# Kernel tuning notes

Measured on AMD Instinct MI355X. Metric: run time of the kernel, lower is better.

The kernel has to match this reference:

```python
import jax, jax.numpy as jnp
import numpy as np


def _conv(x, w, b, pad):
    y = jax.lax.conv_general_dilated(
        x, w, window_strides=(1, 1), padding=[(pad, pad), (pad, pad)],
        dimension_numbers=('NCHW', 'OIHW', 'NCHW'))
    return y + b[None, :, None, None]


def _deform_conv2d(x, offsets, mask, w, b):
    # x: [B,C,H,W]; offsets: [B,2*K,H,W] (dy,dx pairs per kernel tap, row-major taps);
    # mask: [B,K,H,W]; w: [O,C,3,3]; stride=1, padding=1 (torchvision semantics).
    B, C, H, W = x.shape
    K = 9
    off = offsets.reshape(B, K, 2, H, W)
    dy, dx = off[:, :, 0], off[:, :, 1]                      # [B,K,H,W]
    ky = (jnp.arange(K) // 3 - 1).astype(x.dtype)            # tap row offset (pad=1)
    kx = (jnp.arange(K) % 3 - 1).astype(x.dtype)             # tap col offset
    hh = jnp.arange(H, dtype=x.dtype)
    ww = jnp.arange(W, dtype=x.dtype)
    py = hh[None, None, :, None] + ky[None, :, None, None] + dy   # sample y, [B,K,H,W]
    px = ww[None, None, None, :] + kx[None, :, None, None] + dx   # sample x
    y0 = jnp.floor(py); x0 = jnp.floor(px)
    wy = py - y0;      wx = px - x0
    y0i = y0.astype(jnp.int32); x0i = x0.astype(jnp.int32)
    xflat = x.reshape(B, C, H * W)

    def gather(yy, xx):
        # zero padding outside the feature map (torchvision behavior)
        valid = ((yy >= 0) & (yy < H) & (xx >= 0) & (xx < W)).astype(x.dtype)
        idx = jnp.clip(yy, 0, H - 1) * W + jnp.clip(xx, 0, W - 1)
        idx = jnp.broadcast_to(idx.reshape(B, 1, K * H * W), (B, C, K * H * W))
        g = jnp.take_along_axis(xflat, idx, axis=2).reshape(B, C, K, H, W)
        return g * valid[:, None]

    sampled = (gather(y0i, x0i)         * ((1 - wy) * (1 - wx))[:, None]
             + gather(y0i, x0i + 1)     * ((1 - wy) * wx)[:, None]
             + gather(y0i + 1, x0i)     * (wy * (1 - wx))[:, None]
             + gather(y0i + 1, x0i + 1) * (wy * wx)[:, None])       # [B,C,K,H,W]
    sampled = sampled * mask[:, None]                                # modulation
    out = jnp.einsum('bckhw,ock->bohw', sampled, w.reshape(w.shape[0], C, K))
    return out + b[None, :, None, None]


def setup_inputs() -> dict:
    key = jax.random.key(0)
    ks = jax.random.split(key, 5)
    B, C, Ht, Wt, Hs, Ws = 4, 256, 32, 32, 64, 64
    return {
        'template_feat': jax.random.normal(ks[0], (B, C, Ht, Wt), jnp.float32),
        'search_feat':   jax.random.normal(ks[1], (B, C, Hs, Ws), jnp.float32),
        'offset_w': jax.random.normal(ks[2], (18, 2 * C, 3, 3), jnp.float32) * 0.01,
        'offset_b': jnp.zeros((18,), jnp.float32),
        'mask_w':   jax.random.normal(ks[3], (9, 2 * C, 1, 1), jnp.float32) * 0.06,
        'mask_b':   jnp.zeros((9,), jnp.float32),
        'deform_w': jax.random.normal(ks[4], (C, C, 3, 3), jnp.float32) * 0.03,
        'deform_b': jnp.zeros((C,), jnp.float32),
    }


def reference(template_feat, search_feat, offset_w, offset_b, mask_w, mask_b, deform_w, deform_b):
    B, C, Hs, Ws = search_feat.shape
    # F.interpolate(..., mode='bilinear', align_corners=False) == jax half-pixel bilinear
    aligned = jax.image.resize(template_feat, (B, C, Hs, Ws), method='bilinear')
    combined = jnp.concatenate([aligned, search_feat], axis=1)       # [B,2C,H,W]
    offsets = _conv(combined, offset_w, offset_b, 1)                 # [B,18,H,W]
    mask = jax.nn.sigmoid(_conv(combined, mask_w, mask_b, 0))        # [B,9,H,W]
    return _deform_conv2d(search_feat, offsets, mask, deform_w, deform_b)
```

## Files before the change

### kernel.cpp

```cpp
#include <hip/hip_runtime.h>
#include <math.h>

#define BB 4
#define CC 256
#define HH 64
#define WW 64
#define HW 4096
#define XTR 4240
#define XPAD 72

typedef __attribute__((ext_vector_type(8))) _Float16 half8;
typedef __attribute__((ext_vector_type(4))) _Float16 half4;
typedef __attribute__((ext_vector_type(4))) float f32x4;

__device__ inline void gld16(const void* g, void* l) {
    __builtin_amdgcn_global_load_lds((const __attribute__((address_space(1))) void*)g,
                                     (__attribute__((address_space(3))) void*)l, 16, 0, 0);
}

__global__ __launch_bounds__(256) void prep_kernel(
    const float* __restrict__ tmpl, const float* __restrict__ search,
    const float* __restrict__ ow, const float* __restrict__ mw,
    const float* __restrict__ dw,
    _Float16* __restrict__ XT, _Float16* __restrict__ W2, _Float16* __restrict__ W3T) {
    int blk = blockIdx.x;
    int tid = threadIdx.x;
    __shared__ _Float16 ts[64 * 72];

    if (blk < 2048) {
        int ct = blk & 7, y = (blk >> 3) & 63, b = blk >> 9;
        if (ct >= 4) {
            const float* sp = search + ((size_t)(b * CC + (ct - 4) * 64) * HW) + y * 64;
#pragma unroll
            for (int it = 0; it < 4; ++it) {
                int c_l = it * 16 + (tid >> 4);
                int x4 = tid & 15;
                float4 v = *(const float4*)(sp + (size_t)c_l * HW + x4 * 4);
                half4 h;
                h.x = (_Float16)v.x; h.y = (_Float16)v.y;
                h.z = (_Float16)v.z; h.w = (_Float16)v.w;
                *(half4*)&ts[c_l * 72 + x4 * 4] = h;
            }
        } else {
            float sy = 0.5f * (float)y - 0.25f;
            float fy = floorf(sy);
            float wy = sy - fy;
            int y0 = (int)fy;
            int y0c = min(max(y0, 0), 31), y1c = min(max(y0 + 1, 0), 31);
            const float* tp0 = tmpl + ((size_t)(b * CC + ct * 64) * 1024);
            for (int it = 0; it < 16; ++it) {
                int c_l = it * 4 + (tid >> 6);
                int x = tid & 63;
                float sx = 0.5f * (float)x - 0.25f;
                float fx = floorf(sx);
                float wx = sx - fx;
                int x0 = (int)fx;
                int x0c = min(max(x0, 0), 31), x1c = min(max(x0 + 1, 0), 31);
                const float* tp = tp0 + (size_t)c_l * 1024;
                float v00 = tp[y0c * 32 + x0c], v01 = tp[y0c * 32 + x1c];
                float v10 = tp[y1c * 32 + x0c], v11 = tp[y1c * 32 + x1c];
                ts[c_l * 72 + x] = (_Float16)((1.f - wy) * ((1.f - wx) * v00 + wx * v01) +
                                              wy * ((1.f - wx) * v10 + wx * v11));
            }
        }
        __syncthreads();
        size_t rowbase = (size_t)b * XTR + XPAD + (size_t)y * 64;
        for (int it = 0; it < 2; ++it) {
            int idx = it * 256 + tid;
            int x = idx >> 3, w = idx & 7;
            half8 o;
#pragma unroll
            for (int j = 0; j < 8; ++j) o[j] = ts[(w * 8 + j) * 72 + x];
            *(half8*)&XT[(rowbase + x) * 512 + ct * 64 + ((w ^ (x & 7)) * 8)] = o;
        }
    } else if (blk < 2192) {
        int idx = (blk - 2048) * 256 + tid;
        int w = idx & 63;
        int r = (idx >> 6) % 144;
        int b = idx / 9216;
        int pr = (r < 72) ? r : (r + 4096);
        half8 z = {};
        *(half8*)&XT[((size_t)b * XTR + pr) * 512 + w * 8] = z;
    } else if (blk < 2264) {
        int idx = (blk - 2192) * 256 + tid;
        int q = idx & 7;
        int oc = (idx >> 3) & 31;
        int tap = (idx >> 8) % 9;
        int ch = idx / 2304;
        int c0 = ch * 64 + (q ^ (oc & 7)) * 8;
        half8 o;
#pragma unroll
        for (int j = 0; j < 8; ++j) {
            int c = c0 + j;
            float v = 0.f;
            if (oc < 18) v = ow[((size_t)oc * 512 + c) * 9 + tap];
            else if (oc < 27 && tap == 4) v = mw[(size_t)(oc - 18) * 512 + c];
            o[j] = (_Float16)v;
        }
        *(half8*)&W2[(size_t)idx * 8] = o;
    } else {
        int g = (blk - 2264) * 256 + tid;
        int ot = g / 36864;
        int rem = g - ot * 36864;
        int ks = rem >> 9;
        int ci = rem & 511;
        int r = ci >> 2, q = ci & 3;
        int qs = q ^ ((r >> 1) & 3);
        int o_ = ot * 128 + r;
        int kc0 = ks * 32 + qs * 8;
        half8 o;
#pragma unroll
        for (int j = 0; j < 8; ++j) {
            int kc = kc0 + j;
            int k = kc >> 8, c = kc & 255;
            o[j] = (_Float16)dw[((size_t)o_ * CC + c) * 9 + k];
        }
        *(half8*)&W3T[(size_t)g * 8] = o;
    }
}

__global__ __launch_bounds__(256) void offmask_mfma(
    const _Float16* __restrict__ XT, const _Float16* __restrict__ W2,
    const float* __restrict__ ob, const float* __restrict__ mb,
    float* __restrict__ offs, float* __restrict__ maskv) {
    int blk = blockIdx.x;
    int b = blk >> 6, pt = blk & 63;
    int p0 = pt * 64;
    int tid = threadIdx.x, wave = tid >> 6, lane = tid & 63;
    int l15 = lane & 15, kq = lane >> 4;

    __shared__ __align__(16) _Float16 A_s[18432];
    __shared__ __align__(16) _Float16 B_s[12416];

    f32x4 acc[2];
    acc[0] = (f32x4){0.f, 0.f, 0.f, 0.f};
    acc[1] = (f32x4){0.f, 0.f, 0.f, 0.f};

    const char* xrow = (const char*)(XT + ((size_t)b * XTR + XPAD + p0 - 65) * 512);
    half8 z8 = {};
    int x_ = wave * 16 + l15;

    for (int ch = 0; ch < 8; ++ch) {
        __syncthreads();
        const char* srcA = (const char*)W2 + (size_t)ch * 36864;
#pragma unroll
        for (int it = 0; it < 9; ++it) {
            int b16 = it * 256 + wave * 64;
            gld16(srcA + (size_t)(b16 + lane) * 16, (char*)A_s + b16 * 16);
        }
#pragma unroll
        for (int it = 0; it < 7; ++it) {
            int b16 = it * 256 + wave * 64;
            if (b16 < 1552) {
                int c16 = b16 + lane;
                int r_u = c16 >> 3, q = c16 & 7;
                gld16(xrow + (size_t)r_u * 1024 + ch * 128 + q * 16, (char*)B_s + b16 * 16);
            }
        }
        __syncthreads();

#pragma unroll
        for (int tap = 0; tap < 9; ++tap) {
            int ky = tap / 3 - 1, kx = tap % 3 - 1;
            int dlt = ky * 64 + kx;
            int key = (l15 + dlt + 72) & 7;
            bool iv0 = (kx == -1 && x_ == 0) || (kx == 1 && x_ == 63);
            int r0 = wave * 16 + l15 + 65 + dlt;
#pragma unroll
            for (int ks = 0; ks < 2; ++ks) {
                int qa = ((ks * 4 + kq) ^ (l15 & 7)) * 8;
                int qb = ((ks * 4 + kq) ^ key) * 8;
                half8 fa0 = *(const half8*)&A_s[tap * 2048 + l15 * 64 + qa];
                half8 fa1 = *(const half8*)&A_s[tap * 2048 + (16 + l15) * 64 + qa];
                half8 fb0 = *(const half8*)&B_s[r0 * 64 + qb];
                if (iv0) fb0 = z8;
                acc[0] = __builtin_amdgcn_mfma_f32_16x16x32_f16(fa0, fb0, acc[0], 0, 0, 0);
                acc[1] = __builtin_amdgcn_mfma_f32_16x16x32_f16(fa1, fb0, acc[1], 0, 0, 0);
            }
        }
    }

    int px = p0 + x_;
#pragma unroll
    for (int m = 0; m < 2; ++m) {
#pragma unroll
        for (int r = 0; r < 4; ++r) {
            int oc = m * 16 + kq * 4 + r;
            float v = acc[m][r];
            if (oc < 18) {
                offs[(size_t)(b * 18 + oc) * HW + px] = v + ob[oc];
            } else if (oc < 27) {
                float s = v + mb[oc - 18];
                maskv[(size_t)(b * 9 + oc - 18) * HW + px] = 1.f / (1.f + expf(-s));
            }
        }
    }
}

__global__ __launch_bounds__(512) void sample_kernel(
    const _Float16* __restrict__ XT, const float* __restrict__ offs,
    const float* __restrict__ maskv, _Float16* __restrict__ ST2) {
    int blk = blockIdx.x;
    int b = blk >> 7, pt = blk & 127;
    int p0 = pt * 32;
    int tid = threadIdx.x;

    __shared__ ushort4 r4[288];
    __shared__ float4 wg4[288];

    for (int i = tid; i < 288; i += 512) {
        int k = i >> 5, t = i & 31;
        int p = p0 + t;
        int y = p >> 6, x = p & 63;
        float dy = offs[((size_t)(b * 18 + 2 * k)) * HW + p];
        float dx = offs[((size_t)(b * 18 + 2 * k + 1)) * HW + p];
        float m = maskv[((size_t)(b * 9 + k)) * HW + p];
        float py = (float)(y + k / 3 - 1) + dy;
        float px = (float)(x + k % 3 - 1) + dx;
        float fy0 = floorf(py), fx0 = floorf(px);
        float wy = py - fy0, wx = px - fx0;
        int y0 = (int)fy0, x0 = (int)fx0;
        bool vy0 = (y0 >= 0) && (y0 < HH);
        bool vy1 = (y0 + 1 >= 0) && (y0 + 1 < HH);
        bool vx0 = (x0 >= 0) && (x0 < WW);
        bool vx1 = (x0 + 1 >= 0) && (x0 + 1 < WW);
        float w00 = (vy0 && vx0) ? (1.f - wy) * (1.f - wx) * m : 0.f;
        float w01 = (vy0 && vx1) ? (1.f - wy) * wx * m : 0.f;
        float w10 = (vy1 && vx0) ? wy * (1.f - wx) * m : 0.f;
        float w11 = (vy1 && vx1) ? wy * wx * m : 0.f;
        int y0c = min(max(y0, 0), HH - 1), y1c = min(max(y0 + 1, 0), HH - 1);
        int x0c = min(max(x0, 0), WW - 1), x1c = min(max(x0 + 1, 0), WW - 1);
        r4[i] = make_ushort4((ushort)(y0c * 64 + x0c), (ushort)(y0c * 64 + x1c),
                             (ushort)(y1c * 64 + x0c), (ushort)(y1c * 64 + x1c));
        wg4[i] = make_float4(w00, w01, w10, w11);
    }
    __syncthreads();

    const _Float16* xb = XT + ((size_t)b * XTR + XPAD) * 512;
    int oct = tid & 31;
    int gg64 = (4 + (oct >> 3)) * 64;
    int w0 = oct & 7;
    size_t tb = ((size_t)(b * 32 + (pt >> 2))) * 72;

    for (int k = 0; k < 9; ++k) {
        int K0 = k * 256 + oct * 8;
        int ks72 = K0 >> 5;
        int q = oct & 3;
#pragma unroll
        for (int it = 0; it < 2; ++it) {
            int p_l = it * 16 + (tid >> 5);
            ushort4 rr = r4[k * 32 + p_l];
            float4 w = wg4[k * 32 + p_l];
            half8 c00 = *(const half8*)(xb + (size_t)rr.x * 512 + gg64 + ((w0 ^ (rr.x & 7)) * 8));
            half8 c01 = *(const half8*)(xb + (size_t)rr.y * 512 + gg64 + ((w0 ^ (rr.y & 7)) * 8));
            half8 c10 = *(const half8*)(xb + (size_t)rr.z * 512 + gg64 + ((w0 ^ (rr.z & 7)) * 8));
            half8 c11 = *(const half8*)(xb + (size_t)rr.w * 512 + gg64 + ((w0 ^ (rr.w & 7)) * 8));
            half8 o;
#pragma unroll
            for (int j = 0; j < 8; ++j) {
                float v = w.x * (float)c00[j] + w.y * (float)c01[j] +
                          w.z * (float)c10[j] + w.w * (float)c11[j];
                o[j] = (_Float16)v;
            }
            int r = (pt & 3) * 32 + p_l;
            int qs = q ^ ((r >> 1) & 3);
            *(half8*)&ST2[((tb + ks72) << 12) + (r * 4 + qs) * 8] = o;
        }
    }
}

__global__ __launch_bounds__(512) void deform_mfma(
    const _Float16* __restrict__ W3T, const _Float16* __restrict__ ST2,
    const float* __restrict__ db, float* __restrict__ out) {
    int blk = blockIdx.x;
    int b = blk >> 6;
    int ot = (blk >> 5) & 1;
    int pt = blk & 31;
    int o0 = ot * 128, p0 = pt * 128;
    int tid = threadIdx.x;
    int wave = tid >> 6, lane = tid & 63;
    int wo = (wave & 1) * 64, wp = (wave >> 1) * 32;

    __shared__ __align__(16) _Float16 As[4][4096];
    __shared__ __align__(16) _Float16 Bs[4][4096];

    f32x4 acc[4][2];
#pragma unroll
    for (int i = 0; i < 4; ++i)
#pragma unroll
        for (int j = 0; j < 2; ++j) acc[i][j] = (f32x4){0.f, 0.f, 0.f, 0.f};

    const _Float16* Asrc = W3T + (size_t)ot * (72 * 4096);
    const _Float16* Bsrc = ST2 + ((size_t)(b * 32 + pt)) * (72 * 4096);
    int fr = lane & 15, kq8 = lane >> 4;
    int cho = (kq8 ^ ((fr >> 1) & 3)) * 8;

    auto stage = [&](int buf, int ks) {
        gld16(Asrc + (((size_t)ks) << 12) + (size_t)tid * 8,
              (char*)&As[buf][0] + (size_t)tid * 16);
        gld16(Bsrc + (((size_t)ks) << 12) + (size_t)tid * 8,
              (char*)&Bs[buf][0] + (size_t)tid * 16);
    };

    auto compute = [&](int cur) {
        __builtin_amdgcn_s_setprio(1);
        half8 fa[4], fb[2];
#pragma unroll
        for (int f = 0; f < 4; ++f)
            fa[f] = *(const half8*)&As[cur][(wo + f * 16 + fr) * 32 + cho];
#pragma unroll
        for (int g = 0; g < 2; ++g)
            fb[g] = *(const half8*)&Bs[cur][(wp + g * 16 + fr) * 32 + cho];
#pragma unroll
        for (int i = 0; i < 4; ++i)
#pragma unroll
            for (int j = 0; j < 2; ++j)
                acc[i][j] = __builtin_amdgcn_mfma_f32_16x16x32_f16(fa[i], fb[j], acc[i][j], 0, 0, 0);
        __builtin_amdgcn_s_setprio(0);
    };

    stage(0, 0);
    stage(1, 1);
    stage(2, 2);

    for (int m = 0; m < 17; ++m) {
#pragma unroll
        for (int u = 0; u < 4; ++u) {
            int ks = m * 4 + u;
            asm volatile("s_waitcnt vmcnt(4)" ::: "memory");
            __builtin_amdgcn_s_barrier();
            asm volatile("" ::: "memory");
            compute(u);
            stage((u + 3) & 3, ks + 3);
        }
    }
#pragma unroll
    for (int u = 0; u < 4; ++u) {
        int ks = 68 + u;
        if (u < 2)       asm volatile("s_waitcnt vmcnt(4)" ::: "memory");
        else if (u == 2) asm volatile("s_waitcnt vmcnt(2)" ::: "memory");
        else             asm volatile("s_waitcnt vmcnt(0)" ::: "memory");
        __builtin_amdgcn_s_barrier();
        asm volatile("" ::: "memory");
        compute(ks & 3);
        if (u == 0) stage(3, 71);
    }

    int col = lane & 15, rbase = (lane >> 4) * 4;
#pragma unroll
    for (int i = 0; i < 4; ++i) {
        int o_ = o0 + wo + i * 16 + rbase;
#pragma unroll
        for (int j = 0; j < 2; ++j) {
            int p_ = p0 + wp + j * 16 + col;
#pragma unroll
            for (int r = 0; r < 4; ++r) {
                out[((size_t)(b * CC + o_ + r)) * HW + p_] = acc[i][j][r] + db[o_ + r];
            }
        }
    }
}

extern "C" void kernel_launch(void* const* d_in, const int* in_sizes, int n_in,
                              void* d_out, int out_size, void* d_ws, size_t ws_size,
                              hipStream_t stream) {
    const float* tmpl = (const float*)d_in[0];
    const float* search = (const float*)d_in[1];
    const float* ow = (const float*)d_in[2];
    const float* ob = (const float*)d_in[3];
    const float* mw = (const float*)d_in[4];
    const float* mb = (const float*)d_in[5];
    const float* dw = (const float*)d_in[6];
    const float* db = (const float*)d_in[7];
    float* out = (float*)d_out;

    _Float16* XTp = (_Float16*)d_ws;
    _Float16* W2 = XTp + (size_t)4 * XTR * 512;
    _Float16* W3T = W2 + 147456;
    _Float16* ST2 = W3T + 589824;
    float* offsv = (float*)(ST2 + 37748736);
    float* maskv = offsv + 294912;

    prep_kernel<<<2552, 256, 0, stream>>>(tmpl, search, ow, mw, dw, XTp, W2, W3T);
    offmask_mfma<<<256, 256, 0, stream>>>(XTp, W2, ob, mb, offsv, maskv);
    sample_kernel<<<BB * 128, 512, 0, stream>>>(XTp, offsv, maskv, ST2);
    deform_mfma<<<256, 512, 0, stream>>>(W3T, ST2, db, out);
}
```

Measured before the change: 88.12 us.

## Fuse offset/mask conv with bilinear sampling and widen deform GEMM K-step to 64

Merges the offset/mask MFMA kernel and the sampling kernel into one 512-thread kernel. Offsets and masks now stay in shared memory, so the global round-trip and one launch go away. The deform GEMM's K tile is doubled from 32 to 64 per stage, halving the number of barrier/pipeline iterations, and the ST2/W3T layouts and swizzles are reworked to match. The cost is that half the threads sit idle during the conv phase, shared memory use grows (which may lower occupancy), and the fused kernel has only 256 blocks.

```diff
diff --git a/kernel.cpp b/kernel.cpp
--- a/kernel.cpp
+++ b/kernel.cpp
@@ -102,12 +102,12 @@
         int g = (blk - 2264) * 256 + tid;
         int ot = g / 36864;
         int rem = g - ot * 36864;
-        int ks = rem >> 9;
-        int ci = rem & 511;
-        int r = ci >> 2, q = ci & 3;
-        int qs = q ^ ((r >> 1) & 3);
+        int ks = rem >> 10;
+        int ci = rem & 1023;
+        int r = ci >> 3, q = ci & 7;
+        int qs = q ^ (r & 7);
         int o_ = ot * 128 + r;
-        int kc0 = ks * 32 + qs * 8;
+        int kc0 = ks * 64 + qs * 8;
         half8 o;
 #pragma unroll
         for (int j = 0; j < 8; ++j) {
@@ -119,10 +119,10 @@
     }
 }
 
-__global__ __launch_bounds__(256) void offmask_mfma(
+__global__ __launch_bounds__(512) void offsample_kernel(
     const _Float16* __restrict__ XT, const _Float16* __restrict__ W2,
     const float* __restrict__ ob, const float* __restrict__ mb,
-    float* __restrict__ offs, float* __restrict__ maskv) {
+    _Float16* __restrict__ ST2) {
     int blk = blockIdx.x;
     int b = blk >> 6, pt = blk & 63;
     int p0 = pt * 64;
@@ -131,6 +131,9 @@
 
     __shared__ __align__(16) _Float16 A_s[18432];
     __shared__ __align__(16) _Float16 B_s[12416];
+    __shared__ float offs_s[27 * 64];
+    __shared__ ushort4 r4[576];
+    __shared__ float4 wg4[576];
 
     f32x4 acc[2];
     acc[0] = (f32x4){0.f, 0.f, 0.f, 0.f};
@@ -138,83 +141,77 @@
 
     const char* xrow = (const char*)(XT + ((size_t)b * XTR + XPAD + p0 - 65) * 512);
     half8 z8 = {};
-    int x_ = wave * 16 + l15;
+    int x_ = (wave & 3) * 16 + l15;
 
     for (int ch = 0; ch < 8; ++ch) {
         __syncthreads();
-        const char* srcA = (const char*)W2 + (size_t)ch * 36864;
-#pragma unroll
-        for (int it = 0; it < 9; ++it) {
-            int b16 = it * 256 + wave * 64;
-            gld16(srcA + (size_t)(b16 + lane) * 16, (char*)A_s + b16 * 16);
-        }
-#pragma unroll
-        for (int it = 0; it < 7; ++it) {
-            int b16 = it * 256 + wave * 64;
-            if (b16 < 1552) {
-                int c16 = b16 + lane;
-                int r_u = c16 >> 3, q = c16 & 7;
-                gld16(xrow + (size_t)r_u * 1024 + ch * 128 + q * 16, (char*)B_s + b16 * 16);
+        if (tid < 256) {
+            const char* srcA = (const char*)W2 + (size_t)ch * 36864;
+#pragma unroll
+            for (int it = 0; it < 9; ++it) {
+                int b16 = it * 256 + wave * 64;
+                gld16(srcA + (size_t)(b16 + lane) * 16, (char*)A_s + b16 * 16);
+            }
+#pragma unroll
+            for (int it = 0; it < 7; ++it) {
+                int b16 = it * 256 + wave * 64;
+                if (b16 < 1552) {
+                    int c16 = b16 + lane;
+                    int r_u = c16 >> 3, q = c16 & 7;
+                    gld16(xrow + (size_t)r_u * 1024 + ch * 128 + q * 16, (char*)B_s + b16 * 16);
+                }
             }
         }
         __syncthreads();
 
-#pragma unroll
-        for (int tap = 0; tap < 9; ++tap) {
-            int ky = tap / 3 - 1, kx = tap % 3 - 1;
-            int dlt = ky * 64 + kx;
-            int key = (l15 + dlt + 72) & 7;
-            bool iv0 = (kx == -1 && x_ == 0) || (kx == 1 && x_ == 63);
-            int r0 = wave * 16 + l15 + 65 + dlt;
-#pragma unroll
-            for (int ks = 0; ks < 2; ++ks) {
-                int qa = ((ks * 4 + kq) ^ (l15 & 7)) * 8;
-                int qb = ((ks * 4 + kq) ^ key) * 8;
-                half8 fa0 = *(const half8*)&A_s[tap * 2048 + l15 * 64 + qa];
-                half8 fa1 = *(const half8*)&A_s[tap * 2048 + (16 + l15) * 64 + qa];
-                half8 fb0 = *(const half8*)&B_s[r0 * 64 + qb];
-                if (iv0) fb0 = z8;
-                acc[0] = __builtin_amdgcn_mfma_f32_16x16x32_f16(fa0, fb0, acc[0], 0, 0, 0);
-                acc[1] = __builtin_amdgcn_mfma_f32_16x16x32_f16(fa1, fb0, acc[1], 0, 0, 0);
-            }
-        }
-    }
-
-    int px = p0 + x_;
-#pragma unroll
-    for (int m = 0; m < 2; ++m) {
-#pragma unroll
-        for (int r = 0; r < 4; ++r) {
-            int oc = m * 16 + kq * 4 + r;
-            float v = acc[m][r];
-            if (oc < 18) {
-                offs[(size_t)(b * 18 + oc) * HW + px] = v + ob[oc];
-            } else if (oc < 27) {
-                float s = v + mb[oc - 18];
-                maskv[(size_t)(b * 9 + oc - 18) * HW + px] = 1.f / (1.f + expf(-s));
-            }
-        }
-    }
-}
-
-__global__ __launch_bounds__(512) void sample_kernel(
-    const _Float16* __restrict__ XT, const float* __restrict__ offs,
-    const float* __restrict__ maskv, _Float16* __restrict__ ST2) {
-    int blk = blockIdx.x;
-    int b = blk >> 7, pt = blk & 127;
-    int p0 = pt * 32;
-    int tid = threadIdx.x;
-
-    __shared__ ushort4 r4[288];
-    __shared__ float4 wg4[288];
-
-    for (int i = tid; i < 288; i += 512) {
-        int k = i >> 5, t = i & 31;
+        if (tid < 256) {
+#pragma unroll
+            for (int tap = 0; tap < 9; ++tap) {
+                int ky = tap / 3 - 1, kx = tap % 3 - 1;
+                int dlt = ky * 64 + kx;
+                int key = (l15 + dlt + 72) & 7;
+                bool iv0 = (kx == -1 && x_ == 0) || (kx == 1 && x_ == 63);
+                int r0 = wave * 16 + l15 + 65 + dlt;
+#pragma unroll
+                for (int ks = 0; ks < 2; ++ks) {
+                    int qa = ((ks * 4 + kq) ^ (l15 & 7)) * 8;
+                    int qb = ((ks * 4 + kq) ^ key) * 8;
+                    half8 fa0 = *(const half8*)&A_s[tap * 2048 + l15 * 64 + qa];
+                    half8 fa1 = *(const half8*)&A_s[tap * 2048 + (16 + l15) * 64 + qa];
+                    half8 fb0 = *(const half8*)&B_s[r0 * 64 + qb];
+                    if (iv0) fb0 = z8;
+                    acc[0] = __builtin_amdgcn_mfma_f32_16x16x32_f16(fa0, fb0, acc[0], 0, 0, 0);
+                    acc[1] = __builtin_amdgcn_mfma_f32_16x16x32_f16(fa1, fb0, acc[1], 0, 0, 0);
+                }
+            }
+        }
+    }
+
+    if (tid < 256) {
+#pragma unroll
+        for (int m = 0; m < 2; ++m) {
+#pragma unroll
+            for (int r = 0; r < 4; ++r) {
+                int oc = m * 16 + kq * 4 + r;
+                float v = acc[m][r];
+                if (oc < 18) {
+                    offs_s[oc * 64 + x_] = v + ob[oc];
+                } else if (oc < 27) {
+                    float s = v + mb[oc - 18];
+                    offs_s[oc * 64 + x_] = 1.f / (1.f + expf(-s));
+                }
+            }
+        }
+    }
+    __syncthreads();
+
+    for (int i = tid; i < 576; i += 512) {
+        int k = i >> 6, t = i & 63;
         int p = p0 + t;
         int y = p >> 6, x = p & 63;
-        float dy = offs[((size_t)(b * 18 + 2 * k)) * HW + p];
-        float dx = offs[((size_t)(b * 18 + 2 * k + 1)) * HW + p];
-        float m = maskv[((size_t)(b * 9 + k)) * HW + p];
+        float dy = offs_s[(2 * k) * 64 + t];
+        float dx = offs_s[(2 * k + 1) * 64 + t];
+        float m = offs_s[(18 + k) * 64 + t];
         float py = (float)(y + k / 3 - 1) + dy;
         float px = (float)(x + k % 3 - 1) + dx;
         float fy0 = floorf(py), fx0 = floorf(px);
@@ -240,17 +237,16 @@
     int oct = tid & 31;
     int gg64 = (4 + (oct >> 3)) * 64;
     int w0 = oct & 7;
-    size_t tb = ((size_t)(b * 32 + (pt >> 2))) * 72;
+    size_t tb = ((size_t)(b * 32 + (pt >> 1))) * 36;
+    int rbase = (pt & 1) * 64;
 
     for (int k = 0; k < 9; ++k) {
-        int K0 = k * 256 + oct * 8;
-        int ks72 = K0 >> 5;
-        int q = oct & 3;
-#pragma unroll
-        for (int it = 0; it < 2; ++it) {
+        int ks36 = k * 4 + (oct >> 3);
+#pragma unroll
+        for (int it = 0; it < 4; ++it) {
             int p_l = it * 16 + (tid >> 5);
-            ushort4 rr = r4[k * 32 + p_l];
-            float4 w = wg4[k * 32 + p_l];
+            ushort4 rr = r4[k * 64 + p_l];
+            float4 w = wg4[k * 64 + p_l];
             half8 c00 = *(const half8*)(xb + (size_t)rr.x * 512 + gg64 + ((w0 ^ (rr.x & 7)) * 8));
             half8 c01 = *(const half8*)(xb + (size_t)rr.y * 512 + gg64 + ((w0 ^ (rr.y & 7)) * 8));
             half8 c10 = *(const half8*)(xb + (size_t)rr.z * 512 + gg64 + ((w0 ^ (rr.z & 7)) * 8));
@@ -262,9 +258,8 @@
                           w.z * (float)c10[j] + w.w * (float)c11[j];
                 o[j] = (_Float16)v;
             }
-            int r = (pt & 3) * 32 + p_l;
-            int qs = q ^ ((r >> 1) & 3);
-            *(half8*)&ST2[((tb + ks72) << 12) + (r * 4 + qs) * 8] = o;
+            int r = rbase + p_l;
+            *(half8*)&ST2[((tb + ks36) << 13) + (r * 8 + (w0 ^ (r & 7))) * 8] = o;
         }
     }
 }
@@ -281,8 +276,8 @@
     int wave = tid >> 6, lane = tid & 63;
     int wo = (wave & 1) * 64, wp = (wave >> 1) * 32;
 
-    __shared__ __align__(16) _Float16 As[4][4096];
-    __shared__ __align__(16) _Float16 Bs[4][4096];
+    __shared__ __align__(16) _Float16 As[4][8192];
+    __shared__ __align__(16) _Float16 Bs[4][8192];
 
     f32x4 acc[4][2];
 #pragma unroll
@@ -290,32 +285,44 @@
 #pragma unroll
         for (int j = 0; j < 2; ++j) acc[i][j] = (f32x4){0.f, 0.f, 0.f, 0.f};
 
-    const _Float16* Asrc = W3T + (size_t)ot * (72 * 4096);
-    const _Float16* Bsrc = ST2 + ((size_t)(b * 32 + pt)) * (72 * 4096);
+    const _Float16* Asrc = W3T + (size_t)ot * (36 * 8192);
+    const _Float16* Bsrc = ST2 + ((size_t)(b * 32 + pt)) * (36 * 8192);
     int fr = lane & 15, kq8 = lane >> 4;
-    int cho = (kq8 ^ ((fr >> 1) & 3)) * 8;
 
     auto stage = [&](int buf, int ks) {
-        gld16(Asrc + (((size_t)ks) << 12) + (size_t)tid * 8,
-              (char*)&As[buf][0] + (size_t)tid * 16);
-        gld16(Bsrc + (((size_t)ks) << 12) + (size_t)tid * 8,
-              (char*)&Bs[buf][0] + (size_t)tid * 16);
+#pragma unroll
+        for (int t = 0; t < 2; ++t) {
+            int ci = t * 512 + tid;
+            gld16(Asrc + (((size_t)ks) << 13) + (size_t)ci * 8,
+                  (char*)&As[buf][0] + (size_t)ci * 16);
+        }
+#pragma unroll
+        for (int t = 0; t < 2; ++t) {
+            int ci = t * 512 + tid;
+            gld16(Bsrc + (((size_t)ks) << 13) + (size_t)ci * 8,
+                  (char*)&Bs[buf][0] + (size_t)ci * 16);
+        }
     };
 
     auto compute = [&](int cur) {
         __builtin_amdgcn_s_setprio(1);
-        half8 fa[4], fb[2];
-#pragma unroll
-        for (int f = 0; f < 4; ++f)
-            fa[f] = *(const half8*)&As[cur][(wo + f * 16 + fr) * 32 + cho];
-#pragma unroll
-        for (int g = 0; g < 2; ++g)
-            fb[g] = *(const half8*)&Bs[cur][(wp + g * 16 + fr) * 32 + cho];
-#pragma unroll
-        for (int i = 0; i < 4; ++i)
-#pragma unroll
-            for (int j = 0; j < 2; ++j)
-                acc[i][j] = __builtin_amdgcn_mfma_f32_16x16x32_f16(fa[i], fb[j], acc[i][j], 0, 0, 0);
+#pragma unroll
+        for (int ks2 = 0; ks2 < 2; ++ks2) {
+            int c8 = ks2 * 4 + kq8;
+            int cho = (c8 ^ (fr & 7)) * 8;
+            half8 fa[4], fb[2];
+#pragma unroll
+            for (int f = 0; f < 4; ++f)
+                fa[f] = *(const half8*)&As[cur][(wo + f * 16 + fr) * 64 + cho];
+#pragma unroll
+            for (int g = 0; g < 2; ++g)
+                fb[g] = *(const half8*)&Bs[cur][(wp + g * 16 + fr) * 64 + cho];
+#pragma unroll
+            for (int i = 0; i < 4; ++i)
+#pragma unroll
+                for (int j = 0; j < 2; ++j)
+                    acc[i][j] = __builtin_amdgcn_mfma_f32_16x16x32_f16(fa[i], fb[j], acc[i][j], 0, 0, 0);
+        }
         __builtin_amdgcn_s_setprio(0);
     };
 
@@ -323,33 +330,39 @@
     stage(1, 1);
     stage(2, 2);
 
-    for (int m = 0; m < 17; ++m) {
+    for (int m = 0; m < 8; ++m) {
 #pragma unroll
         for (int u = 0; u < 4; ++u) {
             int ks = m * 4 + u;
-            asm volatile("s_waitcnt vmcnt(4)" ::: "memory");
+            asm volatile("s_waitcnt vmcnt(8)" ::: "memory");
             __builtin_amdgcn_s_barrier();
             asm volatile("" ::: "memory");
             compute(u);
             stage((u + 3) & 3, ks + 3);
         }
     }
-#pragma unroll
-    for (int u = 0; u < 4; ++u) {
-        int ks = 68 + u;
-        if (u < 2)       asm volatile("s_waitcnt vmcnt(4)" ::: "memory");
-        else if (u == 2) asm volatile("s_waitcnt vmcnt(2)" ::: "memory");
-        else             asm volatile("s_waitcnt vmcnt(0)" ::: "memory");
-        __builtin_amdgcn_s_barrier();
-        asm volatile("" ::: "memory");
-        compute(ks & 3);
-        if (u == 0) stage(3, 71);
-    }
-
-    int col = lane & 15, rbase = (lane >> 4) * 4;
+    asm volatile("s_waitcnt vmcnt(8)" ::: "memory");
+    __builtin_amdgcn_s_barrier();
+    asm volatile("" ::: "memory");
+    compute(0);
+    stage(3, 35);
+    asm volatile("s_waitcnt vmcnt(8)" ::: "memory");
+    __builtin_amdgcn_s_barrier();
+    asm volatile("" ::: "memory");
+    compute(1);
+    asm volatile("s_waitcnt vmcnt(4)" ::: "memory");
+    __builtin_amdgcn_s_barrier();
+    asm volatile("" ::: "memory");
+    compute(2);
+    asm volatile("s_waitcnt vmcnt(0)" ::: "memory");
+    __builtin_amdgcn_s_barrier();
+    asm volatile("" ::: "memory");
+    compute(3);
+
+    int col = lane & 15, rb = (lane >> 4) * 4;
 #pragma unroll
     for (int i = 0; i < 4; ++i) {
-        int o_ = o0 + wo + i * 16 + rbase;
+        int o_ = o0 + wo + i * 16 + rb;
 #pragma unroll
         for (int j = 0; j < 2; ++j) {
             int p_ = p0 + wp + j * 16 + col;
@@ -378,11 +391,8 @@
     _Float16* W2 = XTp + (size_t)4 * XTR * 512;
     _Float16* W3T = W2 + 147456;
     _Float16* ST2 = W3T + 589824;
-    float* offsv = (float*)(ST2 + 37748736);
-    float* maskv = offsv + 294912;
 
     prep_kernel<<<2552, 256, 0, stream>>>(tmpl, search, ow, mw, dw, XTp, W2, W3T);
-    offmask_mfma<<<256, 256, 0, stream>>>(XTp, W2, ob, mb, offsv, maskv);
-    sample_kernel<<<BB * 128, 512, 0, stream>>>(XTp, offsv, maskv, ST2);
+    offsample_kernel<<<256, 512, 0, stream>>>(XTp, W2, ob, mb, ST2);
     deform_mfma<<<256, 512, 0, stream>>>(W3T, ST2, db, out);
 }
```

New measurement: 82.35 us. 6.6% less time.
